# Kernel tuning notes

Hardware: AMD Instinct MI355X
Metric: run time of the kernel (lower is better)

The kernel has to match this reference:

```python
import jax, jax.numpy as jnp
from jax import lax
import numpy as np

LEVEL_HW = [(100, 100), (50, 50), (25, 25), (13, 13), (7, 7)]  # P3..P7 for 800x800 input
N, C, A, K, NCONV = 2, 256, 9, 80, 4
PRIOR_PROB = 0.01


def conv3x3(x, w, b):
    # x: (N,C,H,W), w: (O,I,3,3), stride 1, pad 1
    y = lax.conv_general_dilated(x, w, (1, 1), 'SAME',
                                 dimension_numbers=('NCHW', 'OIHW', 'NCHW'))
    return y + b[None, :, None, None]


def permute_to_N_HWA_K(t, k):
    # (N, A*k, H, W) -> (N, H*W*A, k), matching the torch helper
    n, _, h, w = t.shape
    return t.reshape(n, -1, k, h, w).transpose(0, 3, 4, 1, 2).reshape(n, -1, k)


def setup_inputs() -> dict:
    key = jax.random.key(0)
    ks = iter(jax.random.split(key, 64))
    inp = {}
    for i, (h, w) in enumerate(LEVEL_HW):
        inp[f"f{i}"] = jax.random.normal(next(ks), (N, C, h, w), jnp.float32)
    for pre in ("cls", "box"):
        for i in range(NCONV):
            inp[f"{pre}_w{i}"] = 0.01 * jax.random.normal(next(ks), (C, C, 3, 3), jnp.float32)
            inp[f"{pre}_b{i}"] = jnp.zeros((C,), jnp.float32)
    bias_value = -float(np.log((1.0 - PRIOR_PROB) / PRIOR_PROB))
    inp["cls_score_w"] = 0.01 * jax.random.normal(next(ks), (A * K, C, 3, 3), jnp.float32)
    inp["cls_score_b"] = jnp.full((A * K,), bias_value, jnp.float32)
    inp["box_pred_w"] = 0.01 * jax.random.normal(next(ks), (A * 4, C, 3, 3), jnp.float32)
    inp["box_pred_b"] = jnp.zeros((A * 4,), jnp.float32)
    return inp


def reference(f0, f1, f2, f3, f4,
              cls_w0, cls_b0, cls_w1, cls_b1, cls_w2, cls_b2, cls_w3, cls_b3,
              box_w0, box_b0, box_w1, box_b1, box_w2, box_b2, box_w3, box_b3,
              cls_score_w, cls_score_b, box_pred_w, box_pred_b):
    feats = [f0, f1, f2, f3, f4]
    cls_p = [(cls_w0, cls_b0), (cls_w1, cls_b1), (cls_w2, cls_b2), (cls_w3, cls_b3)]
    box_p = [(box_w0, box_b0), (box_w1, box_b1), (box_w2, box_b2), (box_w3, box_b3)]
    logits, boxes = [], []
    for f in feats:
        x = f
        for w, b in cls_p:
            x = jax.nn.relu(conv3x3(x, w, b))
        logits.append(permute_to_N_HWA_K(conv3x3(x, cls_score_w, cls_score_b), K))
        y = f
        for w, b in box_p:
            y = jax.nn.relu(conv3x3(y, w, b))
        boxes.append(permute_to_N_HWA_K(conv3x3(y, box_pred_w, box_pred_b), 4))
    # (N, R, K) and (N, R, 4) with R = sum_l Hl*Wl*A = 120087; concat on last dim
    return jnp.concatenate([jnp.concatenate(logits, 1), jnp.concatenate(boxes, 1)], axis=2)
```

## Files before the change

kernel.cpp:

```cpp
#include <hip/hip_runtime.h>


typedef __attribute__((ext_vector_type(8))) short short8;
typedef __attribute__((ext_vector_type(4))) float floatx4;
typedef __attribute__((ext_vector_type(16))) float floatx16;

#define LVLTOT 14143

__device__ __forceinline__ unsigned short f2bf(float f) {
  unsigned int u = __float_as_uint(f);
  unsigned int r = (u + 0x7fffu + ((u >> 16) & 1u)) >> 16;
  return (unsigned short)r;
}

__device__ __forceinline__ void gload_lds16(const void* g, void* l) {
  __builtin_amdgcn_global_load_lds(
      (const __attribute__((address_space(1))) unsigned int*)g,
      (__attribute__((address_space(3))) unsigned int*)l, 16, 0, 0);
}

__global__ __launch_bounds__(256) void border_zero(
    unsigned short* __restrict__ bufA, unsigned short* __restrict__ bufB) {
  static const int Wpt[5] = {102, 52, 27, 15, 9};
  static const int LOFFt[6] = {0, 10404, 13108, 13837, 14062, 14143};
  int idx = blockIdx.x * 256 + threadIdx.x;
  if (idx >= LVLTOT * 32) return;
  int px = idx >> 5, oct = idx & 31;
  int l = 0;
  while (px >= LOFFt[l + 1]) l++;
  int local = px - LOFFt[l];
  int Wp = Wpt[l];
  int r = local / Wp, c = local - r * Wp;
  if (r != 0 && r != Wp - 1 && c != 0 && c != Wp - 1) return;
  int plane = blockIdx.y;
  unsigned short* base = (plane < 4)
                             ? (bufA + (size_t)plane * LVLTOT * 256)
                             : (bufB + (size_t)(plane - 4) * LVLTOT * 256);
  floatx4 z;
  z[0] = z[1] = z[2] = z[3] = 0.f;
  *(floatx4*)(base + (size_t)px * 256 + oct * 8) = z;
}

__global__ __launch_bounds__(256) void xprep(
    const float* __restrict__ f0, const float* __restrict__ f1,
    const float* __restrict__ f2, const float* __restrict__ f3,
    const float* __restrict__ f4, unsigned short* __restrict__ x0) {
  static const int Ht[5] = {100, 50, 25, 13, 7};
  static const int Wpt[5] = {102, 52, 27, 15, 9};
  static const int LOFFt[5] = {0, 10404, 13108, 13837, 14062};
  __shared__ float ts[8][33];
  int bx = blockIdx.x;
  int l, h, wb;
  if (bx < 400)      { l = 0; h = bx >> 2;         wb = bx & 3; }
  else if (bx < 500) { l = 1; h = (bx - 400) >> 1; wb = (bx - 400) & 1; }
  else if (bx < 525) { l = 2; h = bx - 500; wb = 0; }
  else if (bx < 538) { l = 3; h = bx - 525; wb = 0; }
  else               { l = 4; h = bx - 538; wb = 0; }
  const float* f = l == 0 ? f0 : l == 1 ? f1 : l == 2 ? f2 : l == 3 ? f3 : f4;
  int H = Ht[l], W = H, Wp = Wpt[l], loff = LOFFt[l];
  int t = threadIdx.x;
  int w0 = wb * 32;
  int n = blockIdx.z >> 5, cbk = blockIdx.z & 31;
  int cl = t >> 5, wl = t & 31;
  float v = 0.f;
  if (w0 + wl < W)
    v = f[(((size_t)n * 256 + cbk * 8 + cl) * H + h) * W + w0 + wl];
  ts[cl][wl] = v;
  __syncthreads();
  int pi = t >> 3, cj = t & 7;
  if (w0 + pi < W)
    x0[((size_t)n * LVLTOT + loff + (size_t)(h + 1) * Wp + (w0 + pi + 1)) * 256 +
       cbk * 8 + cj] = f2bf(ts[cj][pi]);
}

struct WPArgs {
  const float* src[10];
  unsigned short* dst[10];
  int cout[10];
  int coutp[10];
};
__global__ __launch_bounds__(256) void wprep(WPArgs A) {
  int id = blockIdx.y;
  int idx = blockIdx.x * 256 + threadIdx.x;
  int coutp = A.coutp[id];
  if (idx >= coutp * 256) return;
  int co = idx >> 8, ci = idx & 255;
  const float* w = A.src[id];
  unsigned short* dst = A.dst[id];
  bool valid = co < A.cout[id];
  int cb = co >> 6, cc = (co >> 5) & 1, co32 = co & 31;
  int ch = ci >> 5, ci5 = ci & 31;
  int kk = ci5 >> 4, kh = (ci5 >> 3) & 1, j = ci5 & 7;
#pragma unroll
  for (int tap = 0; tap < 9; tap++) {
    float v = valid ? w[((size_t)co * 256 + ci) * 9 + tap] : 0.f;
    dst[((((size_t)(cb * 8 + ch) * 9 + tap) * 2 + kk) * 2 + cc) * 512 +
        kh * 256 + co32 * 8 + j] = f2bf(v);
  }
}

__device__ __forceinline__ void decode_tile(int tile, int& l, int& h0, int& w0,
                                            int& H, int& W, int& Wp, int& loff) {
  const int Ht[5] = {100, 50, 25, 13, 7};
  const int Wpt[5] = {102, 52, 27, 15, 9};
  const int TXt[5] = {7, 4, 2, 1, 1};
  const int LOFFt[5] = {0, 10404, 13108, 13837, 14062};
  int tloc;
  if (tile < 49) { l = 0; tloc = tile; }
  else if (tile < 65) { l = 1; tloc = tile - 49; }
  else if (tile < 69) { l = 2; tloc = tile - 65; }
  else if (tile < 70) { l = 3; tloc = tile - 69; }
  else { l = 4; tloc = 0; }
  H = Ht[l]; W = H; Wp = Wpt[l]; loff = LOFFt[l];
  int ty = tloc / TXt[l], tx = tloc - ty * TXt[l];
  h0 = ty * 16; w0 = tx * 16;
}

#define CONV_MAIN_LOOP(INP, WBLOB, CB)                                         \
  {                                                                            \
    size_t xoff[6];                                                            \
    _Pragma("unroll") for (int g = 0; g < 6; g++) {                            \
      int px = g * 64 + lane;                                                  \
      int r = px / 18, c = px - r * 18;                                        \
      int hh = h0 + r; if (hh > Hpad - 1) hh = Hpad - 1;                       \
      int ww = w0 + c; if (ww > Wp - 1) ww = Wp - 1;                           \
      xoff[g] = ((size_t)hh * Wp + ww) * 256 + wv * 8;                         \
    }                                                                          \
    for (int ch = 0; ch < 8; ch++) {                                           \
      if (ch) __syncthreads();                                                 \
      const unsigned short* wsrc = (WBLOB) + ((size_t)((CB)*8 + ch)) * 18432;  \
      _Pragma("unroll") for (int i = 0; i < 9; i++)                            \
        gload_lds16(wsrc + i * 2048 + wv * 512 + lane * 8,                     \
                    lds_w + i * 2048 + wv * 512);                              \
      _Pragma("unroll") for (int g = 0; g < 6; g++)                            \
        gload_lds16((INP) + xoff[g] + ch * 32, lds_x + wv * 3072 + g * 512);   \
      __syncthreads();                                                         \
      const short8* xw = (const short8*)lds_w;                                 \
      const short8* xx = (const short8*)lds_x;                                 \
      _Pragma("unroll") for (int tap = 0; tap < 9; tap++) {                    \
        const int tdy = tap / 3, tdx = tap - 3 * (tap / 3);                    \
        short8 bfr[2][2];                                                      \
        _Pragma("unroll") for (int kk = 0; kk < 2; kk++)                       \
          _Pragma("unroll") for (int rr = 0; rr < 2; rr++)                     \
            bfr[kk][rr] = xx[(kk * 2 + kh) * 384 +                             \
                             (wv * 4 + rr * 2 + rh + tdy) * 18 + n15 + tdx];   \
        _Pragma("unroll") for (int kk = 0; kk < 2; kk++)                       \
          _Pragma("unroll") for (int cc = 0; cc < 2; cc++) {                   \
            short8 afr = xw[((tap * 2 + kk) * 2 + cc) * 64 + lane];            \
            _Pragma("unroll") for (int rr = 0; rr < 2; rr++)                   \
              acc[cc][rr] = __builtin_amdgcn_mfma_f32_32x32x16_bf16(           \
                  afr, bfr[kk][rr], acc[cc][rr], 0, 0, 0);                     \
          }                                                                    \
      }                                                                        \
    }                                                                          \
  }

__global__ __launch_bounds__(256, 2) void conv_tower_mfma(
    const unsigned short* __restrict__ xin, unsigned short* __restrict__ xout,
    const unsigned short* __restrict__ wblob_cls,
    const unsigned short* __restrict__ wblob_box,
    const float* __restrict__ bias_cls, const float* __restrict__ bias_box,
    int in_n_stride, int in_tw_stride) {
  __shared__ __align__(16) unsigned short lds_w[18432];
  __shared__ __align__(16) unsigned short lds_x[12288];
  const int t = threadIdx.x, lane = t & 63, wv = t >> 6;
  const int kh = lane >> 5, rh = (lane >> 4) & 1, n15 = lane & 15;
  int l, h0, w0, H, W, Wp, loff;
  decode_tile(blockIdx.x, l, h0, w0, H, W, Wp, loff);
  const int Hpad = H + 2;
  const int cb = blockIdx.y;
  const int n = blockIdx.z >> 1, tw = blockIdx.z & 1;
  const unsigned short* wblob = tw ? wblob_box : wblob_cls;
  const float* bias = tw ? bias_box : bias_cls;
  const unsigned short* inp =
      xin + ((size_t)n * in_n_stride + (size_t)tw * in_tw_stride + loff) * 256;
  unsigned short* outp = xout + ((size_t)(n * 2 + tw) * LVLTOT + loff) * 256;

  floatx16 acc[2][2];
#pragma unroll
  for (int i = 0; i < 2; i++)
#pragma unroll
    for (int jj = 0; jj < 2; jj++)
#pragma unroll
      for (int e = 0; e < 16; e++) acc[i][jj][e] = 0.f;

  CONV_MAIN_LOOP(inp, wblob, cb)

#pragma unroll
  for (int cc = 0; cc < 2; cc++)
#pragma unroll
    for (int r2 = 0; r2 < 4; r2++) {
      int cob = cb * 64 + cc * 32 + 8 * r2 + 4 * kh;
      floatx4 bb = *(const floatx4*)(bias + cob);
#pragma unroll
      for (int rr = 0; rr < 2; rr++) {
        int h = h0 + wv * 4 + rr * 2 + rh;
        int w_ = w0 + n15;
        if (h < H && w_ < W) {
          unsigned short pk[4];
#pragma unroll
          for (int q4 = 0; q4 < 4; q4++)
            pk[q4] = f2bf(fmaxf(acc[cc][rr][r2 * 4 + q4] + bb[q4], 0.f));
          *(unsigned long long*)(outp + ((size_t)(h + 1) * Wp + (w_ + 1)) * 256 +
                                 cob) = *(unsigned long long*)pk;
        }
      }
    }
}

__global__ __launch_bounds__(256, 2) void conv_final_mfma(
    const unsigned short* __restrict__ xin, float* __restrict__ out,
    const unsigned short* __restrict__ wblob_cls,
    const unsigned short* __restrict__ wblob_box,
    const float* __restrict__ bias_cls, const float* __restrict__ bias_box) {
  __shared__ __align__(16) unsigned short lds_w[18432];
  __shared__ __align__(16) unsigned short lds_x[12288];
  const int t = threadIdx.x, lane = t & 63, wv = t >> 6;
  const int kh = lane >> 5, rh = (lane >> 4) & 1, n15 = lane & 15;
  int l, h0, w0, H, W, Wp, loff;
  decode_tile(blockIdx.x, l, h0, w0, H, W, Wp, loff);
  const int Hpad = H + 2;
  const int yb = blockIdx.y;
  const bool is_cls = yb < 12;
  const int cb = is_cls ? yb : 0;
  const int tw = is_cls ? 0 : 1;
  const int Cout = is_cls ? 720 : 36;
  const unsigned short* wblob = is_cls ? wblob_cls : wblob_box;
  const float* bias = is_cls ? bias_cls : bias_box;
  const int n = blockIdx.z;
  const int RB[5] = {0, 90000, 112500, 118125, 119646};
  const unsigned short* inp = xin + ((size_t)(n * 2 + tw) * LVLTOT + loff) * 256;

  floatx16 acc[2][2];
#pragma unroll
  for (int i = 0; i < 2; i++)
#pragma unroll
    for (int jj = 0; jj < 2; jj++)
#pragma unroll
      for (int e = 0; e < 16; e++) acc[i][jj][e] = 0.f;

  CONV_MAIN_LOOP(inp, wblob, cb)

#pragma unroll
  for (int cc = 0; cc < 2; cc++)
#pragma unroll
    for (int r2 = 0; r2 < 4; r2++) {
      int co0 = cb * 64 + cc * 32 + 8 * r2 + 4 * kh;
      if (co0 >= Cout) continue;
      floatx4 bb = *(const floatx4*)(bias + co0);
      int a = is_cls ? (co0 / 80) : (co0 >> 2);
      int col0 = is_cls ? (co0 - a * 80) : 80;
#pragma unroll
      for (int rr = 0; rr < 2; rr++) {
        int h = h0 + wv * 4 + rr * 2 + rh;
        int w_ = w0 + n15;
        if (h < H && w_ < W) {
          size_t ridx = (size_t)RB[l] + ((size_t)h * W + w_) * 9 + a;
          floatx4 v;
#pragma unroll
          for (int q4 = 0; q4 < 4; q4++) v[q4] = acc[cc][rr][r2 * 4 + q4] + bb[q4];
          *(floatx4*)(out + ((size_t)n * 120087 + ridx) * 84 + col0) = v;
        }
      }
    }
}

extern "C" void kernel_launch(void* const* d_in, const int* in_sizes, int n_in,
                              void* d_out, int out_size, void* d_ws,
                              size_t ws_size, hipStream_t stream) {
  char* ws = (char*)d_ws;
  unsigned short* bufB = (unsigned short*)(ws);
  unsigned short* X0 = (unsigned short*)(ws + 14482432);
  unsigned short* bufA = (unsigned short*)(ws + 28964864);
  unsigned short* tb[8];
  for (int i = 0; i < 8; i++)
    tb[i] = (unsigned short*)(ws + 57929728 + (size_t)i * 1179648);
  unsigned short* fb_cls = (unsigned short*)(ws + 67366912);
  unsigned short* fb_box = (unsigned short*)(ws + 70905856);

  float* out = (float*)d_out;

  border_zero<<<dim3((LVLTOT * 32 + 255) / 256, 8), 256, 0, stream>>>(bufA, bufB);
  xprep<<<dim3(545, 1, 64), 256, 0, stream>>>(
      (const float*)d_in[0], (const float*)d_in[1], (const float*)d_in[2],
      (const float*)d_in[3], (const float*)d_in[4], X0);

  WPArgs wa;
  for (int i = 0; i < 4; i++) {
    wa.src[i] = (const float*)d_in[5 + 2 * i];
    wa.src[4 + i] = (const float*)d_in[13 + 2 * i];
    wa.dst[i] = tb[i];
    wa.dst[4 + i] = tb[4 + i];
    wa.cout[i] = wa.cout[4 + i] = 256;
    wa.coutp[i] = wa.coutp[4 + i] = 256;
  }
  wa.src[8] = (const float*)d_in[21]; wa.dst[8] = fb_cls;
  wa.cout[8] = 720; wa.coutp[8] = 768;
  wa.src[9] = (const float*)d_in[23]; wa.dst[9] = fb_box;
  wa.cout[9] = 36; wa.coutp[9] = 64;
  wprep<<<dim3(768, 10), 256, 0, stream>>>(wa);

  const float *cls_b[4], *box_b[4];
  for (int i = 0; i < 4; i++) {
    cls_b[i] = (const float*)d_in[6 + 2 * i];
    box_b[i] = (const float*)d_in[14 + 2 * i];
  }

  dim3 gt(71, 4, 4);
  conv_tower_mfma<<<gt, 256, 0, stream>>>(X0, bufA, tb[0], tb[4], cls_b[0],
                                          box_b[0], LVLTOT, 0);
  conv_tower_mfma<<<gt, 256, 0, stream>>>(bufA, bufB, tb[1], tb[5], cls_b[1],
                                          box_b[1], 2 * LVLTOT, LVLTOT);
  conv_tower_mfma<<<gt, 256, 0, stream>>>(bufB, bufA, tb[2], tb[6], cls_b[2],
                                          box_b[2], 2 * LVLTOT, LVLTOT);
  conv_tower_mfma<<<gt, 256, 0, stream>>>(bufA, bufB, tb[3], tb[7], cls_b[3],
                                          box_b[3], 2 * LVLTOT, LVLTOT);

  conv_final_mfma<<<dim3(71, 13, 2), 256, 0, stream>>>(
      bufB, out, fb_cls, fb_box, (const float*)d_in[22], (const float*)d_in[24]);
}
```

Measured before the change: 707.4 us.

## Switch conv MFMA to 16x16x32, read weights from global, drop weight LDS

Reorders the prepared weight blob so each lane can fetch its A-fragment directly from global memory, removing the weight staging through LDS. The inner loop moves from 32x32x16 to 16x16x32 bf16 MFMAs, with input rows loaded once per dx and reused across the three dy taps. LDS use per block falls to the input tile only, and occupancy is raised to 3 blocks per SM. The cost is that weight reads now go through the cache hierarchy instead of shared LDS, so each wave re-reads the same weights and more global load latency sits in the MFMA loop.

```diff
diff --git a/kernel.cpp b/kernel.cpp
--- a/kernel.cpp
+++ b/kernel.cpp
@@ -3,7 +3,6 @@
 
 typedef __attribute__((ext_vector_type(8))) short short8;
 typedef __attribute__((ext_vector_type(4))) float floatx4;
-typedef __attribute__((ext_vector_type(16))) float floatx16;
 
 #define LVLTOT 14143
 
@@ -87,15 +86,12 @@
   int co = idx >> 8, ci = idx & 255;
   const float* w = A.src[id];
   unsigned short* dst = A.dst[id];
+  int cb = co >> 6, col = co & 63, chk = ci >> 5, qd = (ci >> 3) & 3, j = ci & 7;
   bool valid = co < A.cout[id];
-  int cb = co >> 6, cc = (co >> 5) & 1, co32 = co & 31;
-  int ch = ci >> 5, ci5 = ci & 31;
-  int kk = ci5 >> 4, kh = (ci5 >> 3) & 1, j = ci5 & 7;
 #pragma unroll
   for (int tap = 0; tap < 9; tap++) {
     float v = valid ? w[((size_t)co * 256 + ci) * 9 + tap] : 0.f;
-    dst[((((size_t)(cb * 8 + ch) * 9 + tap) * 2 + kk) * 2 + cc) * 512 +
-        kh * 256 + co32 * 8 + j] = f2bf(v);
+    dst[((((size_t)(cb * 8 + chk) * 9 + tap) * 4 + qd) * 64 + col) * 8 + j] = f2bf(v);
   }
 }
 
@@ -128,43 +124,38 @@
     }                                                                          \
     for (int ch = 0; ch < 8; ch++) {                                           \
       if (ch) __syncthreads();                                                 \
-      const unsigned short* wsrc = (WBLOB) + ((size_t)((CB)*8 + ch)) * 18432;  \
-      _Pragma("unroll") for (int i = 0; i < 9; i++)                            \
-        gload_lds16(wsrc + i * 2048 + wv * 512 + lane * 8,                     \
-                    lds_w + i * 2048 + wv * 512);                              \
       _Pragma("unroll") for (int g = 0; g < 6; g++)                            \
         gload_lds16((INP) + xoff[g] + ch * 32, lds_x + wv * 3072 + g * 512);   \
       __syncthreads();                                                         \
-      const short8* xw = (const short8*)lds_w;                                 \
       const short8* xx = (const short8*)lds_x;                                 \
-      _Pragma("unroll") for (int tap = 0; tap < 9; tap++) {                    \
-        const int tdy = tap / 3, tdx = tap - 3 * (tap / 3);                    \
-        short8 bfr[2][2];                                                      \
-        _Pragma("unroll") for (int kk = 0; kk < 2; kk++)                       \
-          _Pragma("unroll") for (int rr = 0; rr < 2; rr++)                     \
-            bfr[kk][rr] = xx[(kk * 2 + kh) * 384 +                             \
-                             (wv * 4 + rr * 2 + rh + tdy) * 18 + n15 + tdx];   \
-        _Pragma("unroll") for (int kk = 0; kk < 2; kk++)                       \
-          _Pragma("unroll") for (int cc = 0; cc < 2; cc++) {                   \
-            short8 afr = xw[((tap * 2 + kk) * 2 + cc) * 64 + lane];            \
-            _Pragma("unroll") for (int rr = 0; rr < 2; rr++)                   \
-              acc[cc][rr] = __builtin_amdgcn_mfma_f32_32x32x16_bf16(           \
-                  afr, bfr[kk][rr], acc[cc][rr], 0, 0, 0);                     \
+      const short8* wg =                                                       \
+          (const short8*)((WBLOB) + ((size_t)((CB)*8 + ch)) * 18432);          \
+      _Pragma("unroll") for (int tdx = 0; tdx < 3; tdx++) {                    \
+        short8 bfr[6];                                                         \
+        _Pragma("unroll") for (int rw = 0; rw < 6; rw++)                       \
+          bfr[rw] = xx[q * 384 + (wv * 4 + rw) * 18 + n16 + tdx];              \
+        _Pragma("unroll") for (int tdy = 0; tdy < 3; tdy++) {                  \
+          const int tap = tdy * 3 + tdx;                                       \
+          _Pragma("unroll") for (int cc = 0; cc < 4; cc++) {                   \
+            short8 afr = wg[(tap * 4 + q) * 64 + cc * 16 + n16];               \
+            _Pragma("unroll") for (int rr = 0; rr < 4; rr++)                   \
+              acc[cc][rr] = __builtin_amdgcn_mfma_f32_16x16x32_bf16(           \
+                  afr, bfr[rr + tdy], acc[cc][rr], 0, 0, 0);                   \
           }                                                                    \
+        }                                                                      \
       }                                                                        \
     }                                                                          \
   }
 
-__global__ __launch_bounds__(256, 2) void conv_tower_mfma(
+__global__ __launch_bounds__(256, 3) void conv_tower_mfma(
     const unsigned short* __restrict__ xin, unsigned short* __restrict__ xout,
     const unsigned short* __restrict__ wblob_cls,
     const unsigned short* __restrict__ wblob_box,
     const float* __restrict__ bias_cls, const float* __restrict__ bias_box,
     int in_n_stride, int in_tw_stride) {
-  __shared__ __align__(16) unsigned short lds_w[18432];
   __shared__ __align__(16) unsigned short lds_x[12288];
   const int t = threadIdx.x, lane = t & 63, wv = t >> 6;
-  const int kh = lane >> 5, rh = (lane >> 4) & 1, n15 = lane & 15;
+  const int q = lane >> 4, n16 = lane & 15;
   int l, h0, w0, H, W, Wp, loff;
   decode_tile(blockIdx.x, l, h0, w0, H, W, Wp, loff);
   const int Hpad = H + 2;
@@ -176,47 +167,42 @@
       xin + ((size_t)n * in_n_stride + (size_t)tw * in_tw_stride + loff) * 256;
   unsigned short* outp = xout + ((size_t)(n * 2 + tw) * LVLTOT + loff) * 256;
 
-  floatx16 acc[2][2];
-#pragma unroll
-  for (int i = 0; i < 2; i++)
-#pragma unroll
-    for (int jj = 0; jj < 2; jj++)
-#pragma unroll
-      for (int e = 0; e < 16; e++) acc[i][jj][e] = 0.f;
+  floatx4 acc[4][4];
+#pragma unroll
+  for (int i = 0; i < 4; i++)
+#pragma unroll
+    for (int jj = 0; jj < 4; jj++) acc[i][jj] = (floatx4){0.f, 0.f, 0.f, 0.f};
 
   CONV_MAIN_LOOP(inp, wblob, cb)
 
 #pragma unroll
-  for (int cc = 0; cc < 2; cc++)
-#pragma unroll
-    for (int r2 = 0; r2 < 4; r2++) {
-      int cob = cb * 64 + cc * 32 + 8 * r2 + 4 * kh;
-      floatx4 bb = *(const floatx4*)(bias + cob);
-#pragma unroll
-      for (int rr = 0; rr < 2; rr++) {
-        int h = h0 + wv * 4 + rr * 2 + rh;
-        int w_ = w0 + n15;
-        if (h < H && w_ < W) {
-          unsigned short pk[4];
-#pragma unroll
-          for (int q4 = 0; q4 < 4; q4++)
-            pk[q4] = f2bf(fmaxf(acc[cc][rr][r2 * 4 + q4] + bb[q4], 0.f));
-          *(unsigned long long*)(outp + ((size_t)(h + 1) * Wp + (w_ + 1)) * 256 +
-                                 cob) = *(unsigned long long*)pk;
-        }
+  for (int cc = 0; cc < 4; cc++) {
+    floatx4 bb = *(const floatx4*)(bias + cb * 64 + cc * 16 + q * 4);
+#pragma unroll
+    for (int rr = 0; rr < 4; rr++) {
+      int h = h0 + wv * 4 + rr;
+      int w_ = w0 + n16;
+      if (h < H && w_ < W) {
+        unsigned short pk[4];
+#pragma unroll
+        for (int rg = 0; rg < 4; rg++)
+          pk[rg] = f2bf(fmaxf(acc[cc][rr][rg] + bb[rg], 0.f));
+        size_t base =
+            ((size_t)(h + 1) * Wp + (w_ + 1)) * 256 + cb * 64 + cc * 16 + q * 4;
+        *(unsigned long long*)(outp + base) = *(unsigned long long*)pk;
       }
     }
-}
-
-__global__ __launch_bounds__(256, 2) void conv_final_mfma(
+  }
+}
+
+__global__ __launch_bounds__(256, 3) void conv_final_mfma(
     const unsigned short* __restrict__ xin, float* __restrict__ out,
     const unsigned short* __restrict__ wblob_cls,
     const unsigned short* __restrict__ wblob_box,
     const float* __restrict__ bias_cls, const float* __restrict__ bias_box) {
-  __shared__ __align__(16) unsigned short lds_w[18432];
   __shared__ __align__(16) unsigned short lds_x[12288];
   const int t = threadIdx.x, lane = t & 63, wv = t >> 6;
-  const int kh = lane >> 5, rh = (lane >> 4) & 1, n15 = lane & 15;
+  const int q = lane >> 4, n16 = lane & 15;
   int l, h0, w0, H, W, Wp, loff;
   decode_tile(blockIdx.x, l, h0, w0, H, W, Wp, loff);
   const int Hpad = H + 2;
@@ -231,38 +217,34 @@
   const int RB[5] = {0, 90000, 112500, 118125, 119646};
   const unsigned short* inp = xin + ((size_t)(n * 2 + tw) * LVLTOT + loff) * 256;
 
-  floatx16 acc[2][2];
-#pragma unroll
-  for (int i = 0; i < 2; i++)
-#pragma unroll
-    for (int jj = 0; jj < 2; jj++)
-#pragma unroll
-      for (int e = 0; e < 16; e++) acc[i][jj][e] = 0.f;
+  floatx4 acc[4][4];
+#pragma unroll
+  for (int i = 0; i < 4; i++)
+#pragma unroll
+    for (int jj = 0; jj < 4; jj++) acc[i][jj] = (floatx4){0.f, 0.f, 0.f, 0.f};
 
   CONV_MAIN_LOOP(inp, wblob, cb)
 
 #pragma unroll
-  for (int cc = 0; cc < 2; cc++)
-#pragma unroll
-    for (int r2 = 0; r2 < 4; r2++) {
-      int co0 = cb * 64 + cc * 32 + 8 * r2 + 4 * kh;
-      if (co0 >= Cout) continue;
-      floatx4 bb = *(const floatx4*)(bias + co0);
-      int a = is_cls ? (co0 / 80) : (co0 >> 2);
-      int col0 = is_cls ? (co0 - a * 80) : 80;
-#pragma unroll
-      for (int rr = 0; rr < 2; rr++) {
-        int h = h0 + wv * 4 + rr * 2 + rh;
-        int w_ = w0 + n15;
-        if (h < H && w_ < W) {
-          size_t ridx = (size_t)RB[l] + ((size_t)h * W + w_) * 9 + a;
-          floatx4 v;
-#pragma unroll
-          for (int q4 = 0; q4 < 4; q4++) v[q4] = acc[cc][rr][r2 * 4 + q4] + bb[q4];
-          *(floatx4*)(out + ((size_t)n * 120087 + ridx) * 84 + col0) = v;
-        }
+  for (int cc = 0; cc < 4; cc++) {
+    int co0 = cb * 64 + cc * 16 + q * 4;
+    if (co0 >= Cout) continue;
+    floatx4 bb = *(const floatx4*)(bias + co0);
+    int a = is_cls ? (co0 / 80) : (co0 >> 2);
+    int col0 = is_cls ? (co0 - a * 80) : 80;
+#pragma unroll
+    for (int rr = 0; rr < 4; rr++) {
+      int h = h0 + wv * 4 + rr;
+      int w_ = w0 + n16;
+      if (h < H && w_ < W) {
+        size_t ridx = (size_t)RB[l] + ((size_t)h * W + w_) * 9 + a;
+        floatx4 v;
+#pragma unroll
+        for (int rg = 0; rg < 4; rg++) v[rg] = acc[cc][rr][rg] + bb[rg];
+        *(floatx4*)(out + ((size_t)n * 120087 + ridx) * 84 + col0) = v;
       }
     }
+  }
 }
 
 extern "C" void kernel_launch(void* const* d_in, const int* in_sizes, int n_in,
```

After: 1.597 ms. 126% more time.
